# Optimization experiments

Measured on AMD Instinct MI355X. Metric: run time of the kernel, lower is better.

The kernel has to match this reference:

```python
import jax, jax.numpy as jnp
import numpy as np

D = 512; H = 8; HD = D // H; L = 6; QD = 16; MAXLEN = 1000

def _pos_encoding(max_len, d):
    pos = jnp.arange(max_len, dtype=jnp.float32)[:, None]
    div = jnp.exp(jnp.arange(0, d, 2, dtype=jnp.float32) * (-np.log(10000.0) / d))
    pe = jnp.zeros((max_len, d), jnp.float32)
    pe = pe.at[:, 0::2].set(jnp.sin(pos * div))
    pe = pe.at[:, 1::2].set(jnp.cos(pos * div))
    return pe

def _quantum(x, W, b, qwr, qwi, sg, em, mb):
    # QuantumInspiredLayer: classical tanh branch + quantum branch fused by sigmoid gate
    classical = jnp.tanh(x @ W + b)
    qs = x @ sg                          # (B,S,QD) real superposition amplitudes
    ev_r = qs @ qwr                      # complex evolution, real/imag parts kept separate
    ev_i = qs @ qwi
    en_r = ev_r @ em                     # entanglement (real matrix)
    en_i = ev_i @ em
    probs = en_r ** 2 + en_i ** 2        # |entangled|^2, (B,S,QD)
    qout = probs @ mb                    # measurement, (B,S,D)
    fw = jax.nn.sigmoid(jnp.mean(probs, axis=-1, keepdims=True))  # (B,S,1)
    return fw * qout + (1.0 - fw) * classical, probs

def _layer(x, p):
    (Wq, bq, Wk, bk, Wv, bv, Wo, bo,
     qW, qb, qr, qi, qsg, qem, qmb,
     kW, kb, kr, ki, ksg, kem, kmb, g, beta) = p
    B, S, _ = x.shape
    Q = x @ Wq + bq
    K = x @ Wk + bk
    Vv = x @ Wv + bv
    Qq, qp = _quantum(x, qW, qb, qr, qi, qsg, qem, qmb)
    Kq, kp = _quantum(x, kW, kb, kr, ki, ksg, kem, kmb)
    Qf = (0.7 * Q + 0.3 * Qq).reshape(B, S, H, HD).transpose(0, 2, 1, 3)  # (B,H,S,hd)
    Kf = (0.7 * K + 0.3 * Kq).reshape(B, S, H, HD).transpose(0, 2, 1, 3)
    Vh = Vv.reshape(B, S, H, HD).transpose(0, 2, 1, 3)
    scores = jnp.einsum('bhid,bhjd->bhij', Qf, Kf) / np.sqrt(HD).astype(np.float32)
    interf = jnp.einsum('biq,bjq->bij', qp, kp)   # quantum interference term (B,S,S)
    scores = scores + 0.1 * interf[:, None]       # broadcast over heads
    attn = jax.nn.softmax(scores, axis=-1)        # dropout=eval mode (identity)
    ctx = jnp.einsum('bhij,bhjd->bhid', attn, Vh).transpose(0, 2, 1, 3).reshape(B, S, D)
    y = ctx @ Wo + bo + x                         # residual, then LayerNorm
    mu = jnp.mean(y, axis=-1, keepdims=True)
    var = jnp.mean((y - mu) ** 2, axis=-1, keepdims=True)
    y = (y - mu) / jnp.sqrt(var + 1e-5) * g + beta
    return y, attn

def setup_inputs() -> dict:
    key = jax.random.key(0)
    ks = iter(jax.random.split(key, 64))
    def rn(shape, s=0.02):
        return (jax.random.normal(next(ks), shape) * s).astype(jnp.float32)
    B, S, V = 4, 512, 32000
    inp = {
        'text_input': jax.random.randint(next(ks), (B, S), 0, V),
        'visual_input': rn((B, 2048), 1.0),
        'temporal_input': rn((B, 64), 1.0),
        'embed': rn((V, D)),
        'Wvis': rn((2048, D)), 'bvis': jnp.zeros((D,), jnp.float32),
        'Wtemp': rn((64, D)), 'btemp': jnp.zeros((D,), jnp.float32),
        'Wq': rn((L, D, D)), 'bq': jnp.zeros((L, D), jnp.float32),
        'Wk': rn((L, D, D)), 'bk': jnp.zeros((L, D), jnp.float32),
        'Wv': rn((L, D, D)), 'bv': jnp.zeros((L, D), jnp.float32),
        'Wo': rn((L, D, D)), 'bo': jnp.zeros((L, D), jnp.float32),
        'qW': rn((L, D, D)), 'qb': jnp.zeros((L, D), jnp.float32),
        'q_qwr': rn((L, QD, QD), 0.05), 'q_qwi': rn((L, QD, QD), 0.05),
        'q_sg': rn((L, D, QD), 0.05), 'q_em': rn((L, QD, QD), 0.05), 'q_mb': rn((L, QD, D), 0.05),
        'kW': rn((L, D, D)), 'kb': jnp.zeros((L, D), jnp.float32),
        'k_qwr': rn((L, QD, QD), 0.05), 'k_qwi': rn((L, QD, QD), 0.05),
        'k_sg': rn((L, D, QD), 0.05), 'k_em': rn((L, QD, QD), 0.05), 'k_mb': rn((L, QD, D), 0.05),
        'ln_g': jnp.ones((L, D), jnp.float32), 'ln_b': jnp.zeros((L, D), jnp.float32),
        'Ws': rn((D, 64)), 'bs_': jnp.zeros((64,), jnp.float32),
        'Wd': rn((D, 5)), 'bd': jnp.zeros((5,), jnp.float32),
        'We': rn((D, 1)), 'be': jnp.zeros((1,), jnp.float32),
    }
    return inp

def reference(text_input, visual_input, temporal_input, embed, Wvis, bvis, Wtemp, btemp,
              Wq, bq, Wk, bk, Wv, bv, Wo, bo,
              qW, qb, q_qwr, q_qwi, q_sg, q_em, q_mb,
              kW, kb, k_qwr, k_qwi, k_sg, k_em, k_mb,
              ln_g, ln_b, Ws, bs_, Wd, bd, We, be):
    B, S = text_input.shape
    x = (embed[text_input]
         + (visual_input @ Wvis + bvis)[:, None, :]
         + (temporal_input @ Wtemp + btemp)[:, None, :])
    x = x + _pos_encoding(MAXLEN, D)[None, :S, :]
    attns = []
    for l in range(L):
        p = (Wq[l], bq[l], Wk[l], bk[l], Wv[l], bv[l], Wo[l], bo[l],
             qW[l], qb[l], q_qwr[l], q_qwi[l], q_sg[l], q_em[l], q_mb[l],
             kW[l], kb[l], k_qwr[l], k_qwi[l], k_sg[l], k_em[l], k_mb[l],
             ln_g[l], ln_b[l])
        x, a = _layer(x, p)
        attns.append(a)
    pooled = jnp.mean(x, axis=1)  # no attention_mask -> simple mean pool
    skill = jax.nn.sigmoid(pooled @ Ws + bs_)
    diff = jax.nn.softmax(pooled @ Wd + bd, axis=-1)
    eng = jax.nn.sigmoid(pooled @ We + be)
    return skill, diff, eng, x, jnp.stack(attns)
```

## Files before the change

kernel.cpp:

```cpp
#include <hip/hip_runtime.h>
#include <hip/hip_bf16.h>

typedef __attribute__((ext_vector_type(4))) float f32x4;
typedef __attribute__((ext_vector_type(8))) short s16x8;

__device__ __forceinline__ unsigned short f2b(float f) {
  unsigned int u = __float_as_uint(f);
  unsigned int r = (u + 0x7FFFu + ((u >> 16) & 1u)) >> 16;
  return (unsigned short)r;
}
__device__ __forceinline__ float b2f(unsigned short h) {
  return __uint_as_float(((unsigned int)h) << 16);
}
__device__ __forceinline__ void gload16(const void* g, void* l) {
  __builtin_amdgcn_global_load_lds(
      (const __attribute__((address_space(1))) void*)g,
      (__attribute__((address_space(3))) void*)l, 16, 0, 0);
}

enum { MODE_F32 = 0, MODE_VT = 1, MODE_Y = 2, MODE_SC = 3, MODE_CTX = 4 };
struct OutSpec { void* ptr; int mode; };
struct Outs5 { OutSpec o[5]; };
struct Ptr6 { const float* p[6]; };

template<int BM, int BN, int WGM, int WGN>
__global__ __launch_bounds__(256) void gemm_nt(
    const unsigned short* __restrict__ A, int lda, long long strideA,
    const unsigned short* __restrict__ Bm, int ldb, long long strideB,
    const float* __restrict__ biasBase, int biasStride, int perZ,
    Outs5 outs, const float* __restrict__ resid, int K)
{
  constexpr int BK = 32;
  constexpr int WM = BM / WGM, WN = BN / WGN;
  constexpr int WR = WM / 16, WC = WN / 16;
  constexpr int CHA = BM * BK / 8;
  constexpr int CHB = BN * BK / 8;
  __shared__ unsigned short lds_a[2][BM * BK];
  __shared__ unsigned short lds_b[2][BN * BK];
  const int z = blockIdx.z;
  const int tid = threadIdx.x;
  const int wave = tid >> 6, lane = tid & 63;
  const int l16 = lane & 15, lhi = lane >> 4;
  const int wm = (wave / WGN) * WM, wn = (wave % WGN) * WN;
  const int m0 = blockIdx.x * BM, n0 = blockIdx.y * BN;
  const unsigned short* Ap = A + (long long)z * strideA;
  const unsigned short* Bp = Bm + (long long)z * strideB;

  auto stage = [&](int buf, int k0) {
#pragma unroll
    for (int p = 0; p < CHA / 256; ++p) {
      int t = p * 256 + tid;
      gload16(Ap + (long long)(m0 + (t >> 2)) * lda + k0 + (t & 3) * 8,
              &lds_a[buf][t * 8]);
    }
    if constexpr (CHA % 256) {
      if (tid < CHA % 256) {
        int t = (CHA / 256) * 256 + tid;
        gload16(Ap + (long long)(m0 + (t >> 2)) * lda + k0 + (t & 3) * 8,
                &lds_a[buf][t * 8]);
      }
    }
#pragma unroll
    for (int p = 0; p < CHB / 256; ++p) {
      int t = p * 256 + tid;
      gload16(Bp + (long long)(n0 + (t >> 2)) * ldb + k0 + (t & 3) * 8,
              &lds_b[buf][t * 8]);
    }
    if constexpr (CHB % 256) {
      if (tid < CHB % 256) {
        int t = (CHB / 256) * 256 + tid;
        gload16(Bp + (long long)(n0 + (t >> 2)) * ldb + k0 + (t & 3) * 8,
                &lds_b[buf][t * 8]);
      }
    }
  };

  f32x4 acc[WR][WC];
#pragma unroll
  for (int r = 0; r < WR; ++r)
#pragma unroll
    for (int c = 0; c < WC; ++c) { f32x4 zz = {0.f, 0.f, 0.f, 0.f}; acc[r][c] = zz; }

  stage(0, 0);
  __syncthreads();
  int cur = 0;
  for (int k0 = 0; k0 < K; k0 += BK) {
    if (k0 + BK < K) stage(cur ^ 1, k0 + BK);
    s16x8 af[WR], bfv[WC];
#pragma unroll
    for (int r = 0; r < WR; ++r)
      af[r] = *(const s16x8*)&lds_a[cur][(wm + r * 16 + l16) * BK + lhi * 8];
#pragma unroll
    for (int c = 0; c < WC; ++c)
      bfv[c] = *(const s16x8*)&lds_b[cur][(wn + c * 16 + l16) * BK + lhi * 8];
#pragma unroll
    for (int r = 0; r < WR; ++r)
#pragma unroll
      for (int c = 0; c < WC; ++c)
        acc[r][c] = __builtin_amdgcn_mfma_f32_16x16x32_bf16(af[r], bfv[c], acc[r][c], 0, 0, 0);
    __syncthreads();
    cur ^= 1;
  }

  OutSpec spec = perZ ? outs.o[z] : outs.o[0];
  const float* bias = biasBase ? (biasBase + (long long)z * biasStride) : nullptr;
#pragma unroll
  for (int r = 0; r < WR; ++r) {
#pragma unroll
    for (int c = 0; c < WC; ++c) {
      int n = n0 + wn + c * 16 + l16;
      int rb = m0 + wm + r * 16 + lhi * 4;
      float bv = bias ? bias[n] : 0.f;
      float vv[4];
#pragma unroll
      for (int j = 0; j < 4; ++j) vv[j] = acc[r][c][j] + bv;
      if (spec.mode == MODE_F32) {
#pragma unroll
        for (int j = 0; j < 4; ++j)
          ((float*)spec.ptr)[(long long)(rb + j) * 512 + n] = vv[j];
      } else if (spec.mode == MODE_VT) {
        int b = rb >> 9, s = rb & 511;
        ushort4 pk;
        pk.x = f2b(vv[0]); pk.y = f2b(vv[1]); pk.z = f2b(vv[2]); pk.w = f2b(vv[3]);
        *(ushort4*)&((unsigned short*)spec.ptr)[
            (((long long)(b * 8 + (n >> 6))) * 64 + (n & 63)) * 512 + s] = pk;
      } else if (spec.mode == MODE_Y) {
#pragma unroll
        for (int j = 0; j < 4; ++j)
          ((float*)spec.ptr)[(long long)(rb + j) * 512 + n] =
              vv[j] + resid[(long long)(rb + j) * 512 + n];
      } else if (spec.mode == MODE_SC) {
#pragma unroll
        for (int j = 0; j < 4; ++j)
          ((unsigned short*)spec.ptr)[(long long)z * 262144 + (rb + j) * 512 + n] = f2b(vv[j]);
      } else {
        int b = z >> 3, h = z & 7;
#pragma unroll
        for (int j = 0; j < 4; ++j)
          ((unsigned short*)spec.ptr)[((long long)(b * 512 + rb + j)) * 512 + h * 64 + n] = f2b(vv[j]);
      }
    }
  }
}

__global__ __launch_bounds__(256) void wt_k(Ptr6 srcs, unsigned short* __restrict__ wt) {
  __shared__ float tile[32][33];
  int zz = blockIdx.z;
  int l = zz / 6, mat = zz % 6;
  const float* src = srcs.p[mat] + (long long)l * 262144;
  int tx = threadIdx.x, ty = threadIdx.y;
  int n0 = blockIdx.x * 32, k0 = blockIdx.y * 32;
#pragma unroll
  for (int r = 0; r < 4; ++r)
    tile[ty + r * 8][tx] = src[(long long)(k0 + ty + r * 8) * 512 + n0 + tx];
  __syncthreads();
#pragma unroll
  for (int r = 0; r < 4; ++r)
    wt[(long long)zz * 262144 + (long long)(n0 + ty + r * 8) * 512 + k0 + tx] =
        f2b(tile[tx][ty + r * 8]);
}

__global__ __launch_bounds__(256) void prep_k(Ptr6 biases,
    const float* __restrict__ qwr, const float* __restrict__ qwi, const float* __restrict__ qem,
    const float* __restrict__ kwr, const float* __restrict__ kwi, const float* __restrict__ kem,
    float* __restrict__ biasPacked, float* __restrict__ ArAi) {
  int l = blockIdx.x, t = threadIdx.x;
  for (int m = 0; m < 6; ++m)
    for (int d = t; d < 512; d += 256)
      biasPacked[(l * 6 + m) * 512 + d] = biases.p[m][l * 512 + d];
  int i = t >> 4, j = t & 15;
  const float* em0 = qem + l * 256;
  float ar = 0.f, ai = 0.f;
  for (int tt = 0; tt < 16; ++tt) {
    ar += qwr[l * 256 + i * 16 + tt] * em0[tt * 16 + j];
    ai += qwi[l * 256 + i * 16 + tt] * em0[tt * 16 + j];
  }
  ArAi[(l * 4 + 0) * 256 + t] = ar;
  ArAi[(l * 4 + 1) * 256 + t] = ai;
  const float* em1 = kem + l * 256;
  ar = 0.f; ai = 0.f;
  for (int tt = 0; tt < 16; ++tt) {
    ar += kwr[l * 256 + i * 16 + tt] * em1[tt * 16 + j];
    ai += kwi[l * 256 + i * 16 + tt] * em1[tt * 16 + j];
  }
  ArAi[(l * 4 + 2) * 256 + t] = ar;
  ArAi[(l * 4 + 3) * 256 + t] = ai;
}

__global__ __launch_bounds__(512) void vispart_k(const float* __restrict__ vis,
    const float* __restrict__ Wvis, float* __restrict__ part) {
  int b = blockIdx.x, chunk = blockIdx.y, d = threadIdx.x;
  float acc = 0.f;
  for (int k = chunk * 64; k < chunk * 64 + 64; ++k)
    acc += vis[b * 2048 + k] * Wvis[(long long)k * 512 + d];
  part[(b * 32 + chunk) * 512 + d] = acc;
}
__global__ __launch_bounds__(512) void projsum_k(const float* __restrict__ part,
    const float* __restrict__ bvis, const float* __restrict__ temporal,
    const float* __restrict__ Wtemp, const float* __restrict__ btemp, float* __restrict__ proj) {
  int b = blockIdx.x, d = threadIdx.x;
  float acc = bvis[d] + btemp[d];
  for (int c = 0; c < 32; ++c) acc += part[(b * 32 + c) * 512 + d];
  for (int k = 0; k < 64; ++k) acc += temporal[b * 64 + k] * Wtemp[k * 512 + d];
  proj[b * 512 + d] = acc;
}

__global__ __launch_bounds__(512) void embed_k(const int* __restrict__ text,
    const float* __restrict__ emb, const float* __restrict__ proj,
    float* __restrict__ x, unsigned short* __restrict__ xb) {
  int row = blockIdx.x;
  int b = row >> 9, s = row & 511;
  int d = threadIdx.x;
  int tok = text[row];
  float v = emb[(long long)tok * 512 + d] + proj[b * 512 + d];
  float fr = __expf((float)((d >> 1) << 1) * (-9.2103403719761836f / 512.f));
  float ang = (float)s * fr;
  v += (d & 1) ? cosf(ang) : sinf(ang);
  x[(long long)row * 512 + d] = v;
  xb[(long long)row * 512 + d] = f2b(v);
}

__global__ __launch_bounds__(64) void quantum_k(const float* __restrict__ x,
    const float* __restrict__ sg_q, const float* __restrict__ sg_k,
    const float* __restrict__ ArAiL, float* __restrict__ qp, float* __restrict__ kp,
    float* __restrict__ fwq, float* __restrict__ fwk) {
  int row = blockIdx.x, side = blockIdx.y, lane = threadIdx.x;
  const float* sg = side ? sg_k : sg_q;
  const float* Ar = ArAiL + side * 512;
  const float* Ai = Ar + 256;
  float acc[16];
#pragma unroll
  for (int j = 0; j < 16; ++j) acc[j] = 0.f;
  const float* xr = x + (long long)row * 512;
#pragma unroll
  for (int kk = 0; kk < 8; ++kk) {
    float xv = xr[kk * 64 + lane];
    const float* sgr = sg + (kk * 64 + lane) * 16;
#pragma unroll
    for (int j = 0; j < 16; ++j) acc[j] += xv * sgr[j];
  }
#pragma unroll
  for (int s = 32; s; s >>= 1)
#pragma unroll
    for (int j = 0; j < 16; ++j) acc[j] += __shfl_xor(acc[j], s);
  int j = lane & 15;
  float tr = 0.f, ti = 0.f;
#pragma unroll
  for (int t = 0; t < 16; ++t) {
    tr += acc[t] * Ar[t * 16 + j];
    ti += acc[t] * Ai[t * 16 + j];
  }
  float p = tr * tr + ti * ti;
  float ps = p;
#pragma unroll
  for (int s = 1; s < 16; s <<= 1) ps += __shfl_xor(ps, s);
  if (lane < 16) (side ? kp : qp)[row * 16 + lane] = p;
  if (lane == 0) (side ? fwk : fwq)[row] = 1.f / (1.f + __expf(-ps * (1.f / 16.f)));
}

struct FuseP {
  const float* lin; const float* cl; const float* qp; const float* fw;
  const float* mb; unsigned short* ext; float sA, sB;
};
struct Fuse2 { FuseP s[2]; };
__global__ __launch_bounds__(512) void fuse_k(Fuse2 fp) {
  FuseP P = fp.s[blockIdx.y];
  int row = blockIdx.x;
  int b = row >> 9, i = row & 511;
  int d = threadIdx.x;
  const float* qpr = P.qp + row * 16;
  float fwv = P.fw[row];
  float qout = 0.f;
#pragma unroll
  for (int t = 0; t < 16; ++t) qout += qpr[t] * P.mb[t * 512 + d];
  float qq = fwv * qout + (1.f - fwv) * tanhf(P.cl[(long long)row * 512 + d]);
  float val = (0.7f * P.lin[(long long)row * 512 + d] + 0.3f * qq) * P.sA;
  int h = d >> 6, dd = d & 63;
  P.ext[(((long long)(b * 8 + h)) * 512 + i) * 96 + dd] = f2b(val);
  if (d < 128) {
    int h2 = d >> 4, j = d & 15;
    P.ext[(((long long)(b * 8 + h2)) * 512 + i) * 96 + 64 + j] = f2b(P.sB * qpr[j]);
  } else if (d < 256) {
    int t2 = d - 128;
    int h2 = t2 >> 4, j = t2 & 15;
    P.ext[(((long long)(b * 8 + h2)) * 512 + i) * 96 + 80 + j] = 0;
  }
}

__global__ __launch_bounds__(256) void softmax_k(unsigned short* __restrict__ sc,
                                                 float* __restrict__ attn) {
  int wv = threadIdx.x >> 6, lane = threadIdx.x & 63;
  long long row = (long long)blockIdx.x * 4 + wv;
  unsigned short* sp = sc + row * 512 + lane * 8;
  s16x8 v = *(const s16x8*)sp;
  float f[8], mx = -3.4e38f;
#pragma unroll
  for (int j = 0; j < 8; ++j) { f[j] = b2f((unsigned short)v[j]); mx = fmaxf(mx, f[j]); }
#pragma unroll
  for (int s = 32; s; s >>= 1) mx = fmaxf(mx, __shfl_xor(mx, s));
  float e[8], sum = 0.f;
#pragma unroll
  for (int j = 0; j < 8; ++j) { e[j] = __expf(f[j] - mx); sum += e[j]; }
#pragma unroll
  for (int s = 32; s; s >>= 1) sum += __shfl_xor(sum, s);
  float inv = 1.f / sum;
  float* ap = attn + row * 512 + lane * 8;
  f32x4 o0, o1; s16x8 ob;
#pragma unroll
  for (int j = 0; j < 4; ++j) { o0[j] = e[j] * inv; ob[j] = (short)f2b(o0[j]); }
#pragma unroll
  for (int j = 0; j < 4; ++j) { o1[j] = e[4 + j] * inv; ob[4 + j] = (short)f2b(o1[j]); }
  *(f32x4*)ap = o0;
  *(f32x4*)(ap + 4) = o1;
  *(s16x8*)sp = ob;
}

__global__ __launch_bounds__(256) void ln_k(const float* __restrict__ y,
    const float* __restrict__ g, const float* __restrict__ be,
    float* __restrict__ xo, unsigned short* __restrict__ xb, float* __restrict__ xo2) {
  int wv = threadIdx.x >> 6, lane = threadIdx.x & 63;
  long long row = (long long)blockIdx.x * 4 + wv;
  const float* yr = y + row * 512 + lane * 8;
  f32x4 a = *(const f32x4*)yr, b = *(const f32x4*)(yr + 4);
  float s = a[0] + a[1] + a[2] + a[3] + b[0] + b[1] + b[2] + b[3];
#pragma unroll
  for (int m = 32; m; m >>= 1) s += __shfl_xor(s, m);
  float mu = s * (1.f / 512.f);
  float d[8], vs = 0.f;
#pragma unroll
  for (int j = 0; j < 4; ++j) { d[j] = a[j] - mu; vs += d[j] * d[j]; }
#pragma unroll
  for (int j = 0; j < 4; ++j) { d[4 + j] = b[j] - mu; vs += d[4 + j] * d[4 + j]; }
#pragma unroll
  for (int m = 32; m; m >>= 1) vs += __shfl_xor(vs, m);
  float rstd = rsqrtf(vs * (1.f / 512.f) + 1e-5f);
  f32x4 g0 = *(const f32x4*)(g + lane * 8), g1 = *(const f32x4*)(g + lane * 8 + 4);
  f32x4 b0 = *(const f32x4*)(be + lane * 8), b1 = *(const f32x4*)(be + lane * 8 + 4);
  f32x4 o0, o1; s16x8 ob;
#pragma unroll
  for (int j = 0; j < 4; ++j) { o0[j] = d[j] * rstd * g0[j] + b0[j]; ob[j] = (short)f2b(o0[j]); }
#pragma unroll
  for (int j = 0; j < 4; ++j) { o1[j] = d[4 + j] * rstd * g1[j] + b1[j]; ob[4 + j] = (short)f2b(o1[j]); }
  float* xr = xo + row * 512 + lane * 8;
  *(f32x4*)xr = o0; *(f32x4*)(xr + 4) = o1;
  *(s16x8*)(xb + row * 512 + lane * 8) = ob;
  if (xo2) {
    float* x2 = xo2 + row * 512 + lane * 8;
    *(f32x4*)x2 = o0; *(f32x4*)(x2 + 4) = o1;
  }
}

__global__ __launch_bounds__(512) void head_k(const float* __restrict__ x,
    const float* __restrict__ Ws, const float* __restrict__ bs,
    const float* __restrict__ Wd, const float* __restrict__ bd,
    const float* __restrict__ We, const float* __restrict__ be, float* __restrict__ out) {
  __shared__ float pooled[512];
  __shared__ float dl[5];
  int b = blockIdx.x, d = threadIdx.x;
  float s = 0.f;
  for (int t = 0; t < 512; ++t) s += x[((long long)(b * 512 + t)) * 512 + d];
  pooled[d] = s * (1.f / 512.f);
  __syncthreads();
  if (d < 64) {
    float a = bs[d];
    for (int t = 0; t < 512; ++t) a += pooled[t] * Ws[t * 64 + d];
    out[b * 64 + d] = 1.f / (1.f + __expf(-a));
  } else if (d < 69) {
    int j = d - 64;
    float a = bd[j];
    for (int t = 0; t < 512; ++t) a += pooled[t] * Wd[t * 5 + j];
    dl[j] = a;
  } else if (d == 69) {
    float a = be[0];
    for (int t = 0; t < 512; ++t) a += pooled[t] * We[t];
    out[276 + b] = 1.f / (1.f + __expf(-a));
  }
  __syncthreads();
  if (d < 5) {
    float mx = dl[0];
    for (int j = 1; j < 5; ++j) mx = fmaxf(mx, dl[j]);
    float sm = 0.f;
    for (int j = 0; j < 5; ++j) sm += __expf(dl[j] - mx);
    out[256 + b * 5 + d] = __expf(dl[d] - mx) / sm;
  }
}

extern "C" void kernel_launch(void* const* d_in, const int* in_sizes, int n_in,
                              void* d_out, int out_size, void* d_ws, size_t ws_size,
                              hipStream_t stream) {
  (void)in_sizes; (void)n_in; (void)out_size; (void)ws_size;
  const int*   text     = (const int*)  d_in[0];
  const float* visual   = (const float*)d_in[1];
  const float* temporal = (const float*)d_in[2];
  const float* embedw   = (const float*)d_in[3];
  const float* Wvis  = (const float*)d_in[4];  const float* bvis  = (const float*)d_in[5];
  const float* Wtemp = (const float*)d_in[6];  const float* btemp = (const float*)d_in[7];
  const float* Wq = (const float*)d_in[8];   const float* bq = (const float*)d_in[9];
  const float* Wk = (const float*)d_in[10];  const float* bk = (const float*)d_in[11];
  const float* Wv = (const float*)d_in[12];  const float* bv = (const float*)d_in[13];
  const float* Wo = (const float*)d_in[14];  const float* bo = (const float*)d_in[15];
  const float* qW = (const float*)d_in[16];  const float* qb = (const float*)d_in[17];
  const float* q_qwr = (const float*)d_in[18]; const float* q_qwi = (const float*)d_in[19];
  const float* q_sg  = (const float*)d_in[20]; const float* q_em  = (const float*)d_in[21];
  const float* q_mb  = (const float*)d_in[22];
  const float* kW = (const float*)d_in[23];  const float* kb = (const float*)d_in[24];
  const float* k_qwr = (const float*)d_in[25]; const float* k_qwi = (const float*)d_in[26];
  const float* k_sg  = (const float*)d_in[27]; const float* k_em  = (const float*)d_in[28];
  const float* k_mb  = (const float*)d_in[29];
  const float* ln_g = (const float*)d_in[30]; const float* ln_b = (const float*)d_in[31];
  const float* Ws = (const float*)d_in[32];  const float* bs_ = (const float*)d_in[33];
  const float* Wd = (const float*)d_in[34];  const float* bd = (const float*)d_in[35];
  const float* We = (const float*)d_in[36];  const float* be = (const float*)d_in[37];
  float* out = (float*)d_out;

  char* w = (char*)d_ws;
  auto alloc = [&](size_t bytes) {
    char* p = w;
    w += (bytes + 255) & ~(size_t)255;
    return p;
  };
  float* ws_x   = (float*)alloc(2048ll * 512 * 4);
  unsigned short* ws_xb = (unsigned short*)alloc(2048ll * 512 * 2);
  unsigned short* ws_Wt = (unsigned short*)alloc(36ll * 262144 * 2);
  float* ws_bias = (float*)alloc(6ll * 6 * 512 * 4);
  float* ws_ArAi = (float*)alloc(6ll * 1024 * 4);
  float* ws_proj = (float*)alloc(4ll * 512 * 4);
  float* ws_vp   = (float*)alloc(4ll * 32 * 512 * 4);
  float* ws_Q    = (float*)alloc(2048ll * 512 * 4);
  float* ws_K    = (float*)alloc(2048ll * 512 * 4);
  float* ws_Cq   = (float*)alloc(2048ll * 512 * 4);
  float* ws_Ck   = (float*)alloc(2048ll * 512 * 4);
  float* ws_qp   = (float*)alloc(2048ll * 16 * 4);
  float* ws_kp   = (float*)alloc(2048ll * 16 * 4);
  float* ws_fwq  = (float*)alloc(2048ll * 4);
  float* ws_fwk  = (float*)alloc(2048ll * 4);
  unsigned short* ws_Vt   = (unsigned short*)alloc(2048ll * 512 * 2);
  unsigned short* ws_Qext = (unsigned short*)alloc(4ll * 8 * 512 * 96 * 2);
  unsigned short* ws_Kext = (unsigned short*)alloc(4ll * 8 * 512 * 96 * 2);
  unsigned short* ws_sc   = (unsigned short*)alloc(4ll * 8 * 512 * 512 * 2);
  unsigned short* ws_ctx  = (unsigned short*)alloc(2048ll * 512 * 2);
  float* ws_y    = (float*)alloc(2048ll * 512 * 4);

  Ptr6 wsrc = {{Wq, Wk, Wv, qW, kW, Wo}};
  wt_k<<<dim3(16, 16, 36), dim3(32, 8), 0, stream>>>(wsrc, ws_Wt);
  Ptr6 bsrc = {{bq, bk, bv, qb, kb, bo}};
  prep_k<<<dim3(6), dim3(256), 0, stream>>>(bsrc, q_qwr, q_qwi, q_em, k_qwr, k_qwi, k_em,
                                            ws_bias, ws_ArAi);
  vispart_k<<<dim3(4, 32), dim3(512), 0, stream>>>(visual, Wvis, ws_vp);
  projsum_k<<<dim3(4), dim3(512), 0, stream>>>(ws_vp, bvis, temporal, Wtemp, btemp, ws_proj);
  embed_k<<<dim3(2048), dim3(512), 0, stream>>>(text, embedw, ws_proj, ws_x, ws_xb);

  const long long ATTN_OFF = 280ll + 1048576ll;
  for (int l = 0; l < 6; ++l) {
    const unsigned short* WtL = ws_Wt + (long long)l * 6 * 262144;
    const float* biasL = ws_bias + (long long)l * 6 * 512;

    Outs5 o5{};
    o5.o[0] = { ws_Q, MODE_F32 };  o5.o[1] = { ws_K, MODE_F32 };
    o5.o[2] = { ws_Vt, MODE_VT };  o5.o[3] = { ws_Cq, MODE_F32 };
    o5.o[4] = { ws_Ck, MODE_F32 };
    gemm_nt<128, 128, 2, 2><<<dim3(16, 4, 5), 256, 0, stream>>>(
        ws_xb, 512, 0ll, WtL, 512, 262144ll, biasL, 512, 1, o5, nullptr, 512);

    quantum_k<<<dim3(2048, 2), 64, 0, stream>>>(ws_x, q_sg + l * 8192, k_sg + l * 8192,
        ws_ArAi + l * 1024, ws_qp, ws_kp, ws_fwq, ws_fwk);

    Fuse2 f2{};
    f2.s[0] = { ws_Q, ws_Cq, ws_qp, ws_fwq, q_mb + l * 8192, ws_Qext, 0.125f, 0.1f };
    f2.s[1] = { ws_K, ws_Ck, ws_kp, ws_fwk, k_mb + l * 8192, ws_Kext, 1.0f, 1.0f };
    fuse_k<<<dim3(2048, 2), dim3(512), 0, stream>>>(f2);

    Outs5 osc{};
    osc.o[0] = { ws_sc, MODE_SC };
    gemm_nt<128, 128, 2, 2><<<dim3(4, 4, 32), 256, 0, stream>>>(
        ws_Qext, 96, 512ll * 96, ws_Kext, 96, 512ll * 96, nullptr, 0, 0, osc, nullptr, 96);

    float* attnL = out + ATTN_OFF + (long long)l * 8388608;
    softmax_k<<<dim3(4096), dim3(256), 0, stream>>>(ws_sc, attnL);

    Outs5 octx{};
    octx.o[0] = { ws_ctx, MODE_CTX };
    gemm_nt<64, 64, 2, 2><<<dim3(8, 1, 32), 256, 0, stream>>>(
        ws_sc, 512, 262144ll, ws_Vt, 512, 32768ll, nullptr, 0, 0, octx, nullptr, 512);

    Outs5 oy{};
    oy.o[0] = { ws_y, MODE_Y };
    gemm_nt<64, 64, 2, 2><<<dim3(32, 8, 1), 256, 0, stream>>>(
        ws_ctx, 512, 0ll, WtL + 5 * 262144, 512, 0ll, biasL + 5 * 512, 0, 0, oy, ws_x, 512);

    ln_k<<<dim3(512), dim3(256), 0, stream>>>(ws_y, ln_g + l * 512, ln_b + l * 512,
        ws_x, ws_xb, (l == 5) ? (out + 280) : nullptr);
  }

  head_k<<<dim3(4), dim3(512), 0, stream>>>(ws_x, Ws, bs_, Wd, bd, We, be, out);
}
```

Measured before the change: 621.3 us.

## Fuse score GEMM, softmax and context GEMM into one attention kernel

Replaces the three-kernel attention path (QK^T GEMM writing bf16 scores, a separate softmax pass, then the P·V GEMM) with one kernel per (batch·head, 64-row block). That kernel keeps the scores in registers, does the softmax in place, writes the fp32 attention output, and stages bf16 probabilities plus V in swizzled LDS for the context MFMA. This removes the score-buffer round trip through global memory and two kernel launches per layer. The grid drops to 256 blocks with about 110 KB of LDS each and a 128-float accumulator per thread, so occupancy is low. The mean-pool in the head is also split across 32 blocks instead of 4.

```diff
diff --git a/kernel.cpp b/kernel.cpp
--- a/kernel.cpp
+++ b/kernel.cpp
@@ -18,7 +18,7 @@
       (__attribute__((address_space(3))) void*)l, 16, 0, 0);
 }
 
-enum { MODE_F32 = 0, MODE_VT = 1, MODE_Y = 2, MODE_SC = 3, MODE_CTX = 4 };
+enum { MODE_F32 = 0, MODE_VT = 1, MODE_Y = 2 };
 struct OutSpec { void* ptr; int mode; };
 struct Outs5 { OutSpec o[5]; };
 struct Ptr6 { const float* p[6]; };
@@ -50,27 +50,23 @@
 #pragma unroll
     for (int p = 0; p < CHA / 256; ++p) {
       int t = p * 256 + tid;
-      gload16(Ap + (long long)(m0 + (t >> 2)) * lda + k0 + (t & 3) * 8,
-              &lds_a[buf][t * 8]);
+      gload16(Ap + (long long)(m0 + (t >> 2)) * lda + k0 + (t & 3) * 8, &lds_a[buf][t * 8]);
     }
     if constexpr (CHA % 256) {
       if (tid < CHA % 256) {
         int t = (CHA / 256) * 256 + tid;
-        gload16(Ap + (long long)(m0 + (t >> 2)) * lda + k0 + (t & 3) * 8,
-                &lds_a[buf][t * 8]);
+        gload16(Ap + (long long)(m0 + (t >> 2)) * lda + k0 + (t & 3) * 8, &lds_a[buf][t * 8]);
       }
     }
 #pragma unroll
     for (int p = 0; p < CHB / 256; ++p) {
       int t = p * 256 + tid;
-      gload16(Bp + (long long)(n0 + (t >> 2)) * ldb + k0 + (t & 3) * 8,
-              &lds_b[buf][t * 8]);
+      gload16(Bp + (long long)(n0 + (t >> 2)) * ldb + k0 + (t & 3) * 8, &lds_b[buf][t * 8]);
     }
     if constexpr (CHB % 256) {
       if (tid < CHB % 256) {
         int t = (CHB / 256) * 256 + tid;
-        gload16(Bp + (long long)(n0 + (t >> 2)) * ldb + k0 + (t & 3) * 8,
-                &lds_b[buf][t * 8]);
+        gload16(Bp + (long long)(n0 + (t >> 2)) * ldb + k0 + (t & 3) * 8, &lds_b[buf][t * 8]);
       }
     }
   };
@@ -124,21 +120,147 @@
         pk.x = f2b(vv[0]); pk.y = f2b(vv[1]); pk.z = f2b(vv[2]); pk.w = f2b(vv[3]);
         *(ushort4*)&((unsigned short*)spec.ptr)[
             (((long long)(b * 8 + (n >> 6))) * 64 + (n & 63)) * 512 + s] = pk;
-      } else if (spec.mode == MODE_Y) {
+      } else {
 #pragma unroll
         for (int j = 0; j < 4; ++j)
           ((float*)spec.ptr)[(long long)(rb + j) * 512 + n] =
               vv[j] + resid[(long long)(rb + j) * 512 + n];
-      } else if (spec.mode == MODE_SC) {
-#pragma unroll
-        for (int j = 0; j < 4; ++j)
-          ((unsigned short*)spec.ptr)[(long long)z * 262144 + (rb + j) * 512 + n] = f2b(vv[j]);
-      } else {
-        int b = z >> 3, h = z & 7;
-#pragma unroll
-        for (int j = 0; j < 4; ++j)
-          ((unsigned short*)spec.ptr)[((long long)(b * 512 + rb + j)) * 512 + h * 64 + n] = f2b(vv[j]);
       }
+    }
+  }
+}
+
+__global__ __launch_bounds__(256, 1) void fused_attn(
+    const unsigned short* __restrict__ Qe, const unsigned short* __restrict__ Ke,
+    const unsigned short* __restrict__ Vt, float* __restrict__ attn,
+    unsigned short* __restrict__ ctx)
+{
+  __shared__ unsigned short lds[55296];
+  const int z = blockIdx.x, rb = blockIdx.y;
+  const int m0 = rb * 64;
+  const int b = z >> 3, h = z & 7;
+  const int tid = threadIdx.x;
+  const int w = tid >> 6, lane = tid & 63;
+  const int l16 = lane & 15, lhi = lane >> 4;
+  const int rx3 = l16 & 3, rx7 = l16 & 7;
+
+#pragma unroll
+  for (int p = 0; p < 3; ++p) {
+    int t = p * 256 + tid;
+    int row = t / 12, c = t % 12;
+    gload16(Qe + ((long long)(z * 512 + m0 + row)) * 96 + (c ^ (row & 3)) * 8, &lds[t * 8]);
+  }
+#pragma unroll
+  for (int p = 0; p < 24; ++p) {
+    int t = p * 256 + tid;
+    int row = t / 12, c = t % 12;
+    gload16(Ke + ((long long)(z * 512 + row)) * 96 + (c ^ (row & 3)) * 8, &lds[6144 + t * 8]);
+  }
+  __syncthreads();
+
+  const unsigned short* Qs = lds;
+  const unsigned short* Ks = lds + 6144;
+  s16x8 aq[3];
+#pragma unroll
+  for (int kk = 0; kk < 3; ++kk)
+    aq[kk] = *(const s16x8*)&Qs[(w * 16 + l16) * 96 + (kk * 4 + (lhi ^ rx3)) * 8];
+  f32x4 acc[32];
+#pragma unroll
+  for (int c = 0; c < 32; ++c) { f32x4 zz = {0.f, 0.f, 0.f, 0.f}; acc[c] = zz; }
+#pragma unroll
+  for (int c = 0; c < 32; ++c) {
+#pragma unroll
+    for (int kk = 0; kk < 3; ++kk) {
+      s16x8 bf = *(const s16x8*)&Ks[(c * 16 + l16) * 96 + (kk * 4 + (lhi ^ rx3)) * 8];
+      acc[c] = __builtin_amdgcn_mfma_f32_16x16x32_bf16(aq[kk], bf, acc[c], 0, 0, 0);
+    }
+  }
+
+  float inv[4];
+#pragma unroll
+  for (int j = 0; j < 4; ++j) {
+    float mx = acc[0][j];
+#pragma unroll
+    for (int c = 1; c < 32; ++c) mx = fmaxf(mx, acc[c][j]);
+    mx = fmaxf(mx, __shfl_xor(mx, 1));
+    mx = fmaxf(mx, __shfl_xor(mx, 2));
+    mx = fmaxf(mx, __shfl_xor(mx, 4));
+    mx = fmaxf(mx, __shfl_xor(mx, 8));
+    float sum = 0.f;
+#pragma unroll
+    for (int c = 0; c < 32; ++c) { float e = __expf(acc[c][j] - mx); acc[c][j] = e; sum += e; }
+    sum += __shfl_xor(sum, 1);
+    sum += __shfl_xor(sum, 2);
+    sum += __shfl_xor(sum, 4);
+    sum += __shfl_xor(sum, 8);
+    inv[j] = 1.f / sum;
+  }
+  __syncthreads();
+
+#pragma unroll
+  for (int p = 0; p < 8; ++p) {
+    int t = p * 256 + tid;
+    int row = t >> 5, c = t & 31;
+    gload16(Vt + (long long)z * 32768 + row * 512 + (c ^ (row & 7)) * 8, &lds[32768 + t * 8]);
+  }
+  unsigned short* S = lds;
+  {
+    float* ap = attn + (long long)z * 262144;
+#pragma unroll
+    for (int j = 0; j < 4; ++j) {
+      int row_l = w * 16 + lhi * 4 + j;
+      int rs = row_l & 7;
+      float* arow = ap + (long long)(m0 + row_l) * 512;
+      unsigned short* srow = S + row_l * 512;
+#pragma unroll
+      for (int c = 0; c < 32; ++c) {
+        float p = acc[c][j] * inv[j];
+        int col = c * 16 + l16;
+        arow[col] = p;
+        srow[((col >> 3) ^ rs) * 8 + (col & 7)] = f2b(p);
+      }
+    }
+  }
+  __syncthreads();
+
+  const unsigned short* Vl = lds + 32768;
+  f32x4 acc2[4];
+#pragma unroll
+  for (int c2 = 0; c2 < 4; ++c2) { f32x4 zz = {0.f, 0.f, 0.f, 0.f}; acc2[c2] = zz; }
+  const int qrow = w * 16 + l16;
+#pragma unroll
+  for (int kk = 0; kk < 8; ++kk) {
+    s16x8 a = *(const s16x8*)&S[qrow * 512 + ((kk * 4 + lhi) ^ rx7) * 8];
+#pragma unroll
+    for (int c2 = 0; c2 < 4; ++c2) {
+      s16x8 bf = *(const s16x8*)&Vl[(c2 * 16 + l16) * 256 + ((kk * 4 + lhi) ^ rx7) * 8];
+      acc2[c2] = __builtin_amdgcn_mfma_f32_16x16x32_bf16(a, bf, acc2[c2], 0, 0, 0);
+    }
+  }
+  __syncthreads();
+#pragma unroll
+  for (int p = 0; p < 8; ++p) {
+    int t = p * 256 + tid;
+    int row = t >> 5, c = t & 31;
+    gload16(Vt + (long long)z * 32768 + row * 512 + 256 + (c ^ (row & 7)) * 8,
+            &lds[32768 + t * 8]);
+  }
+  __syncthreads();
+#pragma unroll
+  for (int kk = 8; kk < 16; ++kk) {
+    s16x8 a = *(const s16x8*)&S[qrow * 512 + ((kk * 4 + lhi) ^ rx7) * 8];
+#pragma unroll
+    for (int c2 = 0; c2 < 4; ++c2) {
+      s16x8 bf = *(const s16x8*)&Vl[(c2 * 16 + l16) * 256 + (((kk - 8) * 4 + lhi) ^ rx7) * 8];
+      acc2[c2] = __builtin_amdgcn_mfma_f32_16x16x32_bf16(a, bf, acc2[c2], 0, 0, 0);
+    }
+  }
+#pragma unroll
+  for (int c2 = 0; c2 < 4; ++c2) {
+#pragma unroll
+    for (int j = 0; j < 4; ++j) {
+      int row_g = m0 + w * 16 + lhi * 4 + j;
+      ctx[((long long)(b * 512 + row_g)) * 512 + h * 64 + c2 * 16 + l16] = f2b(acc2[c2][j]);
     }
   }
 }
@@ -287,34 +409,6 @@
   }
 }
 
-__global__ __launch_bounds__(256) void softmax_k(unsigned short* __restrict__ sc,
-                                                 float* __restrict__ attn) {
-  int wv = threadIdx.x >> 6, lane = threadIdx.x & 63;
-  long long row = (long long)blockIdx.x * 4 + wv;
-  unsigned short* sp = sc + row * 512 + lane * 8;
-  s16x8 v = *(const s16x8*)sp;
-  float f[8], mx = -3.4e38f;
-#pragma unroll
-  for (int j = 0; j < 8; ++j) { f[j] = b2f((unsigned short)v[j]); mx = fmaxf(mx, f[j]); }
-#pragma unroll
-  for (int s = 32; s; s >>= 1) mx = fmaxf(mx, __shfl_xor(mx, s));
-  float e[8], sum = 0.f;
-#pragma unroll
-  for (int j = 0; j < 8; ++j) { e[j] = __expf(f[j] - mx); sum += e[j]; }
-#pragma unroll
-  for (int s = 32; s; s >>= 1) sum += __shfl_xor(sum, s);
-  float inv = 1.f / sum;
-  float* ap = attn + row * 512 + lane * 8;
-  f32x4 o0, o1; s16x8 ob;
-#pragma unroll
-  for (int j = 0; j < 4; ++j) { o0[j] = e[j] * inv; ob[j] = (short)f2b(o0[j]); }
-#pragma unroll
-  for (int j = 0; j < 4; ++j) { o1[j] = e[4 + j] * inv; ob[4 + j] = (short)f2b(o1[j]); }
-  *(f32x4*)ap = o0;
-  *(f32x4*)(ap + 4) = o1;
-  *(s16x8*)sp = ob;
-}
-
 __global__ __launch_bounds__(256) void ln_k(const float* __restrict__ y,
     const float* __restrict__ g, const float* __restrict__ be,
     float* __restrict__ xo, unsigned short* __restrict__ xb, float* __restrict__ xo2) {
@@ -350,7 +444,14 @@
   }
 }
 
-__global__ __launch_bounds__(512) void head_k(const float* __restrict__ x,
+__global__ __launch_bounds__(512) void poolpart_k(const float* __restrict__ x,
+                                                   float* __restrict__ part) {
+  int b = blockIdx.x, ch = blockIdx.y, d = threadIdx.x;
+  float s = 0.f;
+  for (int r = 0; r < 64; ++r) s += x[((long long)(b * 512 + ch * 64 + r)) * 512 + d];
+  part[(b * 8 + ch) * 512 + d] = s;
+}
+__global__ __launch_bounds__(512) void head_k(const float* __restrict__ part,
     const float* __restrict__ Ws, const float* __restrict__ bs,
     const float* __restrict__ Wd, const float* __restrict__ bd,
     const float* __restrict__ We, const float* __restrict__ be, float* __restrict__ out) {
@@ -358,7 +459,7 @@
   __shared__ float dl[5];
   int b = blockIdx.x, d = threadIdx.x;
   float s = 0.f;
-  for (int t = 0; t < 512; ++t) s += x[((long long)(b * 512 + t)) * 512 + d];
+  for (int t = 0; t < 8; ++t) s += part[(b * 8 + t) * 512 + d];
   pooled[d] = s * (1.f / 512.f);
   __syncthreads();
   if (d < 64) {
@@ -437,7 +538,6 @@
   unsigned short* ws_Vt   = (unsigned short*)alloc(2048ll * 512 * 2);
   unsigned short* ws_Qext = (unsigned short*)alloc(4ll * 8 * 512 * 96 * 2);
   unsigned short* ws_Kext = (unsigned short*)alloc(4ll * 8 * 512 * 96 * 2);
-  unsigned short* ws_sc   = (unsigned short*)alloc(4ll * 8 * 512 * 512 * 2);
   unsigned short* ws_ctx  = (unsigned short*)alloc(2048ll * 512 * 2);
   float* ws_y    = (float*)alloc(2048ll * 512 * 4);
 
@@ -470,18 +570,8 @@
     f2.s[1] = { ws_K, ws_Ck, ws_kp, ws_fwk, k_mb + l * 8192, ws_Kext, 1.0f, 1.0f };
     fuse_k<<<dim3(2048, 2), dim3(512), 0, stream>>>(f2);
 
-    Outs5 osc{};
-    osc.o[0] = { ws_sc, MODE_SC };
-    gemm_nt<128, 128, 2, 2><<<dim3(4, 4, 32), 256, 0, stream>>>(
-        ws_Qext, 96, 512ll * 96, ws_Kext, 96, 512ll * 96, nullptr, 0, 0, osc, nullptr, 96);
-
-    float* attnL = out + ATTN_OFF + (long long)l * 8388608;
-    softmax_k<<<dim3(4096), dim3(256), 0, stream>>>(ws_sc, attnL);
-
-    Outs5 octx{};
-    octx.o[0] = { ws_ctx, MODE_CTX };
-    gemm_nt<64, 64, 2, 2><<<dim3(8, 1, 32), 256, 0, stream>>>(
-        ws_sc, 512, 262144ll, ws_Vt, 512, 32768ll, nullptr, 0, 0, octx, nullptr, 512);
+    fused_attn<<<dim3(32, 8), 256, 0, stream>>>(
+        ws_Qext, ws_Kext, ws_Vt, out + ATTN_OFF + (long long)l * 8388608, ws_ctx);
 
     Outs5 oy{};
     oy.o[0] = { ws_y, MODE_Y };
@@ -492,5 +582,6 @@
         ws_x, ws_xb, (l == 5) ? (out + 280) : nullptr);
   }
 
-  head_k<<<dim3(4), dim3(512), 0, stream>>>(ws_x, Ws, bs_, Wd, bd, We, be, out);
-}
+  poolpart_k<<<dim3(4, 8), dim3(512), 0, stream>>>(ws_x, ws_vp);
+  head_k<<<dim3(4), dim3(512), 0, stream>>>(ws_vp, Ws, bs_, Wd, bd, We, be, out);
+}
```

Measured after the change: 507.8 us (median of 3 runs). -18.3%, faster.
